# Performance work log

Measured on AMD Instinct MI355X. Metric: run time of the kernel, lower is better.

## Reference

```python
import jax, jax.numpy as jnp
import numpy as np

H = 768       # hidden_size
NH = 12       # num_attention_heads
HD = H // NH  # head_size
FF = 3072     # intermediate_size
EPS = 1e-5


def _layernorm(x, g, b):
    m = jnp.mean(x, axis=-1, keepdims=True)
    v = jnp.var(x, axis=-1, keepdims=True)
    return (x - m) * jax.lax.rsqrt(v + EPS) * g + b


def setup_inputs() -> dict:
    key = jax.random.key(0)
    ks = jax.random.split(key, 12)
    B, Sq, Skv = 8, 1024, 1024
    s = 0.02
    return {
        "freq_hidden_states": jax.random.normal(ks[0], (B, Sq, H), jnp.float32),
        "image_hidden_states": jax.random.normal(ks[1], (B, Skv, H), jnp.float32),
        # attention projections (stored [in, out])
        "Wq": jax.random.normal(ks[2], (H, H), jnp.float32) * s,
        "bq": jnp.zeros((H,), jnp.float32),
        "Wk": jax.random.normal(ks[3], (H, H), jnp.float32) * s,
        "bk": jnp.zeros((H,), jnp.float32),
        "Wv": jax.random.normal(ks[4], (H, H), jnp.float32) * s,
        "bv": jnp.zeros((H,), jnp.float32),
        # layernorms
        "ln_att_g": jnp.ones((H,), jnp.float32),
        "ln_att_b": jnp.zeros((H,), jnp.float32),
        "ln_mlp_g": jnp.ones((H,), jnp.float32),
        "ln_mlp_b": jnp.zeros((H,), jnp.float32),
        # MLP
        "W1": jax.random.normal(ks[5], (H, FF), jnp.float32) * s,
        "b1": jnp.zeros((FF,), jnp.float32),
        "W2": jax.random.normal(ks[6], (FF, H), jnp.float32) * s,
        "b2": jnp.zeros((H,), jnp.float32),
    }


def reference(image_hidden_states, freq_hidden_states, Wq, bq, Wk, bk, Wv, bv,
              ln_att_g, ln_att_b, ln_mlp_g, ln_mlp_b, W1, b1, W2, b2):
    B, Sq, _ = freq_hidden_states.shape
    Skv = image_hidden_states.shape[1]
    # cross-attention: query from freq, key/value from image
    q = (freq_hidden_states @ Wq + bq).reshape(B, Sq, NH, HD)
    k = (image_hidden_states @ Wk + bk).reshape(B, Skv, NH, HD)
    v = (image_hidden_states @ Wv + bv).reshape(B, Skv, NH, HD)
    scores = jnp.einsum("bqhd,bkhd->bhqk", q, k) / jnp.sqrt(jnp.float32(HD))
    probs = jax.nn.softmax(scores, axis=-1)
    ctx = jnp.einsum("bhqk,bkhd->bqhd", probs, v).reshape(B, Sq, H)
    # residual with post-LN on the attention output
    h = freq_hidden_states + _layernorm(ctx, ln_att_g, ln_att_b)
    # MLP + residual with post-LN on the MLP output
    mlp = jax.nn.relu(h @ W1 + b1) @ W2 + b2
    return h + _layernorm(mlp, ln_mlp_g, ln_mlp_b)
```

## Files before the change

kernel.cpp:

```cpp
#include <hip/hip_runtime.h>
#include <hip/hip_bf16.h>

#define H 768
#define NH 12
#define HD 64
#define FF 3072
#define SQ 1024
#define SKV 1024

typedef __hip_bfloat16 bf16;
typedef __attribute__((ext_vector_type(8))) short short8;
typedef __attribute__((ext_vector_type(4))) float f32x4;

__device__ inline void gload16(const void* g, void* l) {
  __builtin_amdgcn_global_load_lds((const __attribute__((address_space(1))) void*)g,
                                   (__attribute__((address_space(3))) void*)l, 16, 0, 0);
}

__device__ inline float bf2f(unsigned short u) {
  unsigned int x = ((unsigned int)u) << 16;
  return __builtin_bit_cast(float, x);
}

__device__ inline void cvt_body(const float* __restrict__ src, bf16* __restrict__ dst, int blk) {
  int i = blk * 256 + threadIdx.x;
  float4 v = ((const float4*)src)[i];
  union { unsigned short u[4]; uint2 q; } o;
  bf16 t0 = __float2bfloat16(v.x); o.u[0] = *(unsigned short*)&t0;
  bf16 t1 = __float2bfloat16(v.y); o.u[1] = *(unsigned short*)&t1;
  bf16 t2 = __float2bfloat16(v.z); o.u[2] = *(unsigned short*)&t2;
  bf16 t3 = __float2bfloat16(v.w); o.u[3] = *(unsigned short*)&t3;
  ((uint2*)dst)[i] = o.q;
}

__device__ inline void trans_body(const float* __restrict__ src, bf16* __restrict__ dst,
                                  int Kd, int Nd, int blk, float* tile ) {
  int ntx = Nd >> 5;
  int n0 = (blk % ntx) << 5, k0 = (blk / ntx) << 5;
  int tx = threadIdx.x & 31, ty = threadIdx.x >> 5;
#pragma unroll
  for (int i = 0; i < 4; ++i)
    tile[(ty + i * 8) * 33 + tx] = src[(size_t)(k0 + ty + i * 8) * Nd + n0 + tx];
  __syncthreads();
#pragma unroll
  for (int i = 0; i < 4; ++i)
    dst[(size_t)(n0 + ty + i * 8) * Kd + k0 + tx] = __float2bfloat16(tile[tx * 33 + ty + i * 8]);
}

__global__ __launch_bounds__(256) void prep(
    const float* freq, const float* image, bf16* freqb, bf16* imageb,
    const float* Wq, const float* Wk, const float* Wv, const float* W1, const float* W2,
    bf16* WTq, bf16* WTk, bf16* WTv, bf16* W1T, bf16* W2T, int c1) {
  __shared__ float tile[32 * 33];
  int b = blockIdx.x;
  if (b < c1) { cvt_body(freq, freqb, b); return; }
  b -= c1;
  if (b < c1) { cvt_body(image, imageb, b); return; }
  b -= c1;
  const int TQ = (H / 32) * (H / 32);
  const int T1 = (FF / 32) * (H / 32);
  if (b < TQ)            { trans_body(Wq, WTq, H, H, b, tile); return; }
  b -= TQ;
  if (b < TQ)            { trans_body(Wk, WTk, H, H, b, tile); return; }
  b -= TQ;
  if (b < TQ)            { trans_body(Wv, WTv, H, H, b, tile); return; }
  b -= TQ;
  if (b < T1)            { trans_body(W1, W1T, H, FF, b, tile); return; }
  b -= T1;
  trans_body(W2, W2T, FF, H, b, tile);
}

template <int EPI, int BN>
__global__ __launch_bounds__(256) void gemm_bt(
    const bf16* __restrict__ A, const bf16* __restrict__ BT,
    const float* __restrict__ bias0, const float* __restrict__ bias1,
    void* __restrict__ out0, void* __restrict__ out1, int M, int N, int K) {
  constexpr int SI = BN / 32;
  constexpr int JF = BN / 32;
  __shared__ __align__(16) bf16 lA[128 * 64];
  __shared__ __align__(16) bf16 lB[BN * 64];
  const int t = threadIdx.x;
  const int lane = t & 63, w = t >> 6;
  const int wr = w >> 1, wc = w & 1;
  const int nt = N / BN;
  const int nwg = gridDim.x;
  int bid = blockIdx.x;
  int logical = ((nwg & 7) == 0) ? ((bid & 7) * (nwg >> 3) + (bid >> 3)) : bid;
  const int m0 = (logical / nt) << 7;
  const int n0 = (logical % nt) * BN;

  const f32x4 fz = {0.f, 0.f, 0.f, 0.f};
  f32x4 acc[4][JF];
#pragma unroll
  for (int i = 0; i < 4; ++i)
#pragma unroll
    for (int j = 0; j < JF; ++j) acc[i][j] = fz;

  for (int kt = 0; kt < K; kt += 64) {
#pragma unroll
    for (int i = 0; i < 4; ++i) {
      int idx = i * 256 + t;
      int row = idx >> 3;
      int chunk = (idx & 7) ^ (row & 7);
      gload16(A + (size_t)(m0 + row) * K + kt + chunk * 8, lA + (size_t)(i * 256 + w * 64) * 8);
    }
#pragma unroll
    for (int i = 0; i < SI; ++i) {
      int idx = i * 256 + t;
      int row = idx >> 3;
      int chunk = (idx & 7) ^ (row & 7);
      gload16(BT + (size_t)(n0 + row) * K + kt + chunk * 8, lB + (size_t)(i * 256 + w * 64) * 8);
    }
    __syncthreads();

    short8 af[2][4], bfv[2][JF];
#pragma unroll
    for (int s = 0; s < 2; ++s) {
#pragma unroll
      for (int i = 0; i < 4; ++i) {
        int ra = wr * 64 + i * 16 + (lane & 15);
        int ca = (s * 4 + (lane >> 4)) ^ (ra & 7);
        af[s][i] = *(const short8*)&lA[ra * 64 + ca * 8];
      }
#pragma unroll
      for (int j = 0; j < JF; ++j) {
        int rb = wc * (BN / 2) + j * 16 + (lane & 15);
        int cb = (s * 4 + (lane >> 4)) ^ (rb & 7);
        bfv[s][j] = *(const short8*)&lB[rb * 64 + cb * 8];
      }
    }
#pragma unroll
    for (int s = 0; s < 2; ++s)
#pragma unroll
      for (int i = 0; i < 4; ++i)
#pragma unroll
        for (int j = 0; j < JF; ++j)
          acc[i][j] = __builtin_amdgcn_mfma_f32_16x16x32_bf16(af[s][i], bfv[s][j], acc[i][j], 0, 0, 0);
    __syncthreads();
  }

#pragma unroll
  for (int i = 0; i < 4; ++i) {
    int mbase = m0 + wr * 64 + i * 16 + ((lane >> 4) << 2);
#pragma unroll
    for (int j = 0; j < JF; ++j) {
      int n = n0 + wc * (BN / 2) + j * 16 + (lane & 15);
#pragma unroll
      for (int r = 0; r < 4; ++r) {
        int m = mbase + r;
        float v = acc[i][j][r];
        if (EPI == 0) {
          v = (v + bias0[n]) * 0.180336880f;
          int hlin = (m >> 10) * NH + (n >> 6);
          ((bf16*)out0)[((size_t)hlin * SQ + (m & 1023)) * HD + (n & 63)] = __float2bfloat16(v);
        } else if (EPI == 1) {
          int sel = (n >= H);
          int nn = n - (sel ? H : 0);
          v += (sel ? bias1 : bias0)[nn];
          int hlin = (m >> 10) * NH + (nn >> 6);
          if (!sel)
            ((bf16*)out0)[((size_t)hlin * SKV + (m & 1023)) * HD + (nn & 63)] = __float2bfloat16(v);
          else
            ((bf16*)out1)[((size_t)hlin * HD + (nn & 63)) * SKV + (m & 1023)] = __float2bfloat16(v);
        } else if (EPI == 2) {
          v += bias0[n];
          v = fmaxf(v, 0.f);
          ((bf16*)out0)[(size_t)m * N + n] = __float2bfloat16(v);
        } else {
          v += bias0[n];
          ((bf16*)out0)[(size_t)m * N + n] = __float2bfloat16(v);
        }
      }
    }
  }
}

__global__ __launch_bounds__(512, 4) void attn_fwd(
    const bf16* __restrict__ Q,
    const bf16* __restrict__ Kg_,
    const bf16* __restrict__ VT,
    bf16* __restrict__ ctx, int nblk) {
  __shared__ __align__(16) bf16 Ks[2][64 * 64];
  __shared__ __align__(16) bf16 Vs[2][64 * 64];
  __shared__ __align__(16) bf16 PQ[8 * 16 * 72];

  const int t = threadIdx.x, lane = t & 63, w = t >> 6;
  int bid = blockIdx.x;
  int logical = ((nblk & 7) == 0) ? (bid & 7) * (nblk >> 3) + (bid >> 3) : bid;
  const int hl = logical >> 3;
  const int q0 = (logical & 7) << 7;
  const bf16* Qg = Q + ((size_t)hl * SQ + q0) * HD;
  const bf16* Kg = Kg_ + (size_t)hl * SKV * HD;
  const bf16* Vg = VT + (size_t)hl * HD * SKV;

#pragma unroll
  for (int rep = 0; rep < 2; ++rep) {
    int idx = rep * 512 + t;
    int row = idx >> 3;
    int chunk = (idx & 7) ^ (row & 7);
    gload16(Qg + (size_t)row * HD + chunk * 8, PQ + (size_t)(rep * 512 + w * 64) * 8);
  }
  {
    int row = t >> 3, chunk = (t & 7) ^ (row & 7);
    gload16(Kg + (size_t)row * HD + chunk * 8, &Ks[0][(size_t)w * 64 * 8]);
    gload16(Vg + (size_t)row * SKV + chunk * 8, &Vs[0][(size_t)w * 64 * 8]);
  }
  __syncthreads();

  short8 aq[2];
#pragma unroll
  for (int s = 0; s < 2; ++s) {
    int row = w * 16 + (lane & 15);
    int chunk = (s * 4 + (lane >> 4)) ^ (row & 7);
    aq[s] = *(const short8*)&PQ[row * 64 + chunk * 8];
  }
  __syncthreads();

  float l_r[4];
#pragma unroll
  for (int r = 0; r < 4; ++r) l_r[r] = 0.f;
  const f32x4 fz = {0.f, 0.f, 0.f, 0.f};
  f32x4 oacc[4];
#pragma unroll
  for (int j = 0; j < 4; ++j) oacc[j] = fz;

  bf16* Pw = PQ + w * (16 * 72);
  const short s1 = (short)0x3F80;
  const short8 ones = {s1, s1, s1, s1, s1, s1, s1, s1};

#pragma unroll 2
  for (int i = 0; i < 16; ++i) {
    const int buf = i & 1;
    if (i < 15) {
      int kvn = (i + 1) << 6;
      int row = t >> 3, chunk = (t & 7) ^ (row & 7);
      gload16(Kg + (size_t)(kvn + row) * HD + chunk * 8, &Ks[buf ^ 1][(size_t)w * 64 * 8]);
      gload16(Vg + (size_t)row * SKV + kvn + chunk * 8, &Vs[buf ^ 1][(size_t)w * 64 * 8]);
    }

    f32x4 sa[4];
#pragma unroll
    for (int n = 0; n < 4; ++n) sa[n] = fz;
    __builtin_amdgcn_s_setprio(1);
#pragma unroll
    for (int s = 0; s < 2; ++s)
#pragma unroll
      for (int n = 0; n < 4; ++n) {
        int rb = n * 16 + (lane & 15);
        int cb = (s * 4 + (lane >> 4)) ^ (rb & 7);
        short8 bk = *(const short8*)&Ks[buf][rb * 64 + cb * 8];
        sa[n] = __builtin_amdgcn_mfma_f32_16x16x32_bf16(aq[s], bk, sa[n], 0, 0, 0);
      }
    __builtin_amdgcn_s_setprio(0);

#pragma unroll
    for (int n = 0; n < 4; ++n)
#pragma unroll
      for (int r = 0; r < 4; ++r)
        Pw[(((lane >> 4) << 2) + r) * 72 + n * 16 + (lane & 15)] =
            __float2bfloat16(exp2f(sa[n][r]));

    f32x4 ld = fz;
    __builtin_amdgcn_s_setprio(1);
#pragma unroll
    for (int kk = 0; kk < 2; ++kk) {
      short8 pa = *(const short8*)&Pw[(lane & 15) * 72 + kk * 32 + ((lane >> 4) << 3)];
      ld = __builtin_amdgcn_mfma_f32_16x16x32_bf16(pa, ones, ld, 0, 0, 0);
#pragma unroll
      for (int j = 0; j < 4; ++j) {
        int rb = j * 16 + (lane & 15);
        int cb = (kk * 4 + (lane >> 4)) ^ (rb & 7);
        short8 bv = *(const short8*)&Vs[buf][rb * 64 + cb * 8];
        oacc[j] = __builtin_amdgcn_mfma_f32_16x16x32_bf16(pa, bv, oacc[j], 0, 0, 0);
      }
    }
    __builtin_amdgcn_s_setprio(0);
#pragma unroll
    for (int r = 0; r < 4; ++r) l_r[r] += ld[r];

    __syncthreads();
  }

  const int b = hl / NH, hh = hl % NH;
  float rl[4];
#pragma unroll
  for (int r = 0; r < 4; ++r) rl[r] = 1.0f / l_r[r];
#pragma unroll
  for (int j = 0; j < 4; ++j)
#pragma unroll
    for (int r = 0; r < 4; ++r) {
      int q = q0 + w * 16 + ((lane >> 4) << 2) + r;
      int d = j * 16 + (lane & 15);
      ctx[((size_t)b * SQ + q) * H + hh * HD + d] = __float2bfloat16(oacc[j][r] * rl[r]);
    }
}

__global__ __launch_bounds__(256) void ln_res(
    const bf16* __restrict__ x, const float* __restrict__ res,
    const float* __restrict__ g, const float* __restrict__ beta,
    float* __restrict__ o32, bf16* __restrict__ ob, int write_b) {
  const int row = blockIdx.x;
  const int t = threadIdx.x;
  float v[4];
  float s = 0.f, s2 = 0.f;
  if (t < 192) {
    ushort4 xv = ((const ushort4*)(x + (size_t)row * H))[t];
    v[0] = bf2f(xv.x); v[1] = bf2f(xv.y); v[2] = bf2f(xv.z); v[3] = bf2f(xv.w);
#pragma unroll
    for (int k = 0; k < 4; ++k) { s += v[k]; s2 += v[k] * v[k]; }
  } else {
#pragma unroll
    for (int k = 0; k < 4; ++k) v[k] = 0.f;
  }
#pragma unroll
  for (int off = 32; off > 0; off >>= 1) {
    s += __shfl_down(s, off);
    s2 += __shfl_down(s2, off);
  }
  __shared__ float red[8];
  if ((t & 63) == 0) { red[t >> 6] = s; red[4 + (t >> 6)] = s2; }
  __syncthreads();
  float st = red[0] + red[1] + red[2] + red[3];
  float s2t = red[4] + red[5] + red[6] + red[7];
  float mean = st * (1.f / 768.f);
  float var = s2t * (1.f / 768.f) - mean * mean;
  float rs = rsqrtf(var + 1e-5f);
  if (t < 192) {
    float4 rv = ((const float4*)(res + (size_t)row * H))[t];
    float4 gv = ((const float4*)g)[t];
    float4 bv = ((const float4*)beta)[t];
    float4 o;
    o.x = rv.x + (v[0] - mean) * rs * gv.x + bv.x;
    o.y = rv.y + (v[1] - mean) * rs * gv.y + bv.y;
    o.z = rv.z + (v[2] - mean) * rs * gv.z + bv.z;
    o.w = rv.w + (v[3] - mean) * rs * gv.w + bv.w;
    ((float4*)(o32 + (size_t)row * H))[t] = o;
    if (write_b) {
      union { unsigned short u[4]; uint2 q; } ob4;
      bf16 b0 = __float2bfloat16(o.x); ob4.u[0] = *(unsigned short*)&b0;
      bf16 b1 = __float2bfloat16(o.y); ob4.u[1] = *(unsigned short*)&b1;
      bf16 b2 = __float2bfloat16(o.z); ob4.u[2] = *(unsigned short*)&b2;
      bf16 b3 = __float2bfloat16(o.w); ob4.u[3] = *(unsigned short*)&b3;
      ((uint2*)(ob + (size_t)row * H))[t] = ob4.q;
    }
  }
}

extern "C" void kernel_launch(void* const* d_in, const int* in_sizes, int n_in,
                              void* d_out, int out_size, void* d_ws, size_t ws_size,
                              hipStream_t stream) {
  const float* freq  = (const float*)d_in[0];
  const float* image = (const float*)d_in[1];
  const float* Wq = (const float*)d_in[2];
  const float* bq = (const float*)d_in[3];
  const float* Wk = (const float*)d_in[4];
  const float* bk = (const float*)d_in[5];
  const float* Wv = (const float*)d_in[6];
  const float* bv = (const float*)d_in[7];
  const float* g1 = (const float*)d_in[8];
  const float* be1 = (const float*)d_in[9];
  const float* g2 = (const float*)d_in[10];
  const float* be2 = (const float*)d_in[11];
  const float* W1 = (const float*)d_in[12];
  const float* b1 = (const float*)d_in[13];
  const float* W2 = (const float*)d_in[14];
  const float* b2 = (const float*)d_in[15];

  const int Bc = in_sizes[0] / (SQ * H);
  const int M = Bc * SQ;

  char* p = (char*)d_ws;
  bf16* W1T = (bf16*)p;  p += (size_t)FF * H * 2;
  bf16* W2T = (bf16*)p;  p += (size_t)H * FF * 2;
  bf16* ctxb = (bf16*)p; p += (size_t)M * H * 2;
  float* h32 = (float*)p; p += (size_t)M * H * 4;
  bf16* hb = (bf16*)p;   p += (size_t)M * H * 2;
  char* U = p;
  bf16* freqb = (bf16*)U;
  bf16* imageb = (bf16*)(U + (size_t)M * H * 2);
  bf16* WTq   = (bf16*)(U + (size_t)2 * M * H * 2);
  bf16* WTkv  = (bf16*)(U + (size_t)2 * M * H * 2 + (size_t)H * H * 2);
  bf16* Qb    = (bf16*)(U + (size_t)2 * M * H * 2 + (size_t)3 * H * H * 2);
  bf16* Kbuf  = (bf16*)((char*)Qb + (size_t)M * H * 2);
  bf16* VTb   = (bf16*)((char*)Kbuf + (size_t)M * H * 2);
  bf16* mlp1  = (bf16*)U;
  bf16* mlp2b = ctxb;

  int c1 = M * H / 1024;
  int nprep = 2 * c1 + 3 * ((H / 32) * (H / 32)) + (FF / 32) * (H / 32) + (H / 32) * (FF / 32);
  prep<<<nprep, 256, 0, stream>>>(freq, image, freqb, imageb,
                                  Wq, Wk, Wv, W1, W2,
                                  WTq, WTkv, WTkv + (size_t)H * H, W1T, W2T, c1);

  gemm_bt<0, 64><<<(M / 128) * (H / 64), 256, 0, stream>>>(freqb, WTq, bq, nullptr, Qb, nullptr, M, H, H);
  gemm_bt<1, 128><<<(M / 128) * (2 * H / 128), 256, 0, stream>>>(imageb, WTkv, bk, bv, Kbuf, VTb, M, 2 * H, H);
  int nblk = Bc * NH * (SQ / 128);
  attn_fwd<<<nblk, 512, 0, stream>>>(Qb, Kbuf, VTb, ctxb, nblk);
  ln_res<<<M, 256, 0, stream>>>(ctxb, freq, g1, be1, h32, hb, 1);
  gemm_bt<2, 128><<<(M / 128) * (FF / 128), 256, 0, stream>>>(hb, W1T, b1, nullptr, mlp1, nullptr, M, FF, H);
  gemm_bt<3, 64><<<(M / 128) * (H / 64), 256, 0, stream>>>(mlp1, W2T, b2, nullptr, mlp2b, nullptr, M, H, FF);
  ln_res<<<M, 256, 0, stream>>>(mlp2b, h32, g2, be2, (float*)d_out, nullptr, 0);
}
```

Before: 246.8 us.

## Rewrite attention with 32x32 MFMA, register-resident P via permlane swap

The attention kernel moves from 8 waves of 16x16x32 MFMA to 4 waves of 32x32x16 MFMA, each wave owning 32 query rows. It computes S^T so the exp'd probabilities can be packed to bf16 with v_cvt_pk and rearranged with v_permlane32_swap into PV operands, removing the LDS round-trip for P. Row sums are accumulated with scalar adds instead of an extra MFMA against ones. This cuts LDS traffic and MFMA instruction count but halves threads per block and raises register pressure per wave.

```diff
diff --git a/kernel.cpp b/kernel.cpp
--- a/kernel.cpp
+++ b/kernel.cpp
@@ -11,6 +11,7 @@
 typedef __hip_bfloat16 bf16;
 typedef __attribute__((ext_vector_type(8))) short short8;
 typedef __attribute__((ext_vector_type(4))) float f32x4;
+typedef __attribute__((ext_vector_type(16))) float f32x16;
 
 __device__ inline void gload16(const void* g, void* l) {
   __builtin_amdgcn_global_load_lds((const __attribute__((address_space(1))) void*)g,
@@ -20,6 +21,12 @@
 __device__ inline float bf2f(unsigned short u) {
   unsigned int x = ((unsigned int)u) << 16;
   return __builtin_bit_cast(float, x);
+}
+
+__device__ inline unsigned int cvtpk(float lo, float hi) {
+  unsigned int r;
+  asm("v_cvt_pk_bf16_f32 %0, %1, %2" : "=v"(r) : "v"(lo), "v"(hi));
+  return r;
 }
 
 __device__ inline void cvt_body(const float* __restrict__ src, bf16* __restrict__ dst, int blk) {
@@ -175,16 +182,17 @@
   }
 }
 
-__global__ __launch_bounds__(512, 4) void attn_fwd(
+__global__ __launch_bounds__(256) void attn_fwd(
     const bf16* __restrict__ Q,
     const bf16* __restrict__ Kg_,
     const bf16* __restrict__ VT,
     bf16* __restrict__ ctx, int nblk) {
+  __shared__ __align__(16) bf16 Qs[128 * 64];
   __shared__ __align__(16) bf16 Ks[2][64 * 64];
   __shared__ __align__(16) bf16 Vs[2][64 * 64];
-  __shared__ __align__(16) bf16 PQ[8 * 16 * 72];
 
   const int t = threadIdx.x, lane = t & 63, w = t >> 6;
+  const int hi = lane >> 5, l31 = lane & 31;
   int bid = blockIdx.x;
   int logical = ((nblk & 7) == 0) ? (bid & 7) * (nblk >> 3) + (bid >> 3) : bid;
   const int hl = logical >> 3;
@@ -194,105 +202,119 @@
   const bf16* Vg = VT + (size_t)hl * HD * SKV;
 
 #pragma unroll
+  for (int rep = 0; rep < 4; ++rep) {
+    int slot = rep * 256 + t;
+    int row = slot >> 3, chunk = (slot & 7) ^ (row & 7);
+    gload16(Qg + (size_t)row * HD + chunk * 8, (char*)Qs + (size_t)slot * 16);
+  }
+#pragma unroll
   for (int rep = 0; rep < 2; ++rep) {
-    int idx = rep * 512 + t;
-    int row = idx >> 3;
-    int chunk = (idx & 7) ^ (row & 7);
-    gload16(Qg + (size_t)row * HD + chunk * 8, PQ + (size_t)(rep * 512 + w * 64) * 8);
-  }
-  {
-    int row = t >> 3, chunk = (t & 7) ^ (row & 7);
-    gload16(Kg + (size_t)row * HD + chunk * 8, &Ks[0][(size_t)w * 64 * 8]);
-    gload16(Vg + (size_t)row * SKV + chunk * 8, &Vs[0][(size_t)w * 64 * 8]);
+    int slot = rep * 256 + t;
+    int row = slot >> 3, chunk = (slot & 7) ^ (row & 7);
+    gload16(Kg + (size_t)row * HD + chunk * 8, (char*)&Ks[0][0] + (size_t)slot * 16);
+    gload16(Vg + (size_t)row * SKV + chunk * 8, (char*)&Vs[0][0] + (size_t)slot * 16);
   }
   __syncthreads();
 
-  short8 aq[2];
-#pragma unroll
-  for (int s = 0; s < 2; ++s) {
-    int row = w * 16 + (lane & 15);
-    int chunk = (s * 4 + (lane >> 4)) ^ (row & 7);
-    aq[s] = *(const short8*)&PQ[row * 64 + chunk * 8];
-  }
-  __syncthreads();
-
-  float l_r[4];
-#pragma unroll
-  for (int r = 0; r < 4; ++r) l_r[r] = 0.f;
-  const f32x4 fz = {0.f, 0.f, 0.f, 0.f};
-  f32x4 oacc[4];
-#pragma unroll
-  for (int j = 0; j < 4; ++j) oacc[j] = fz;
-
-  bf16* Pw = PQ + w * (16 * 72);
-  const short s1 = (short)0x3F80;
-  const short8 ones = {s1, s1, s1, s1, s1, s1, s1, s1};
+  short8 aq[4];
+#pragma unroll
+  for (int ks = 0; ks < 4; ++ks) {
+    int row = w * 32 + l31;
+    int chunk = (ks * 2 + hi) ^ (row & 7);
+    aq[ks] = *(const short8*)&Qs[row * 64 + chunk * 8];
+  }
+
+  f32x16 oa0, oa1;
+#pragma unroll
+  for (int r = 0; r < 16; ++r) { oa0[r] = 0.f; oa1[r] = 0.f; }
+  float ls0 = 0.f, ls1 = 0.f;
 
 #pragma unroll 2
   for (int i = 0; i < 16; ++i) {
     const int buf = i & 1;
     if (i < 15) {
       int kvn = (i + 1) << 6;
-      int row = t >> 3, chunk = (t & 7) ^ (row & 7);
-      gload16(Kg + (size_t)(kvn + row) * HD + chunk * 8, &Ks[buf ^ 1][(size_t)w * 64 * 8]);
-      gload16(Vg + (size_t)row * SKV + kvn + chunk * 8, &Vs[buf ^ 1][(size_t)w * 64 * 8]);
-    }
-
-    f32x4 sa[4];
-#pragma unroll
-    for (int n = 0; n < 4; ++n) sa[n] = fz;
+#pragma unroll
+      for (int rep = 0; rep < 2; ++rep) {
+        int slot = rep * 256 + t;
+        int row = slot >> 3, chunk = (slot & 7) ^ (row & 7);
+        gload16(Kg + (size_t)(kvn + row) * HD + chunk * 8, (char*)&Ks[buf ^ 1][0] + (size_t)slot * 16);
+        gload16(Vg + (size_t)row * SKV + kvn + chunk * 8, (char*)&Vs[buf ^ 1][0] + (size_t)slot * 16);
+      }
+    }
+
+    f32x16 sc0, sc1;
+#pragma unroll
+    for (int r = 0; r < 16; ++r) { sc0[r] = 0.f; sc1[r] = 0.f; }
     __builtin_amdgcn_s_setprio(1);
 #pragma unroll
-    for (int s = 0; s < 2; ++s)
-#pragma unroll
-      for (int n = 0; n < 4; ++n) {
-        int rb = n * 16 + (lane & 15);
-        int cb = (s * 4 + (lane >> 4)) ^ (rb & 7);
-        short8 bk = *(const short8*)&Ks[buf][rb * 64 + cb * 8];
-        sa[n] = __builtin_amdgcn_mfma_f32_16x16x32_bf16(aq[s], bk, sa[n], 0, 0, 0);
+    for (int ks = 0; ks < 4; ++ks) {
+      int c0 = ks * 2 + hi;
+      int r0 = l31;
+      short8 kf0 = *(const short8*)&Ks[buf][r0 * 64 + (c0 ^ (r0 & 7)) * 8];
+      sc0 = __builtin_amdgcn_mfma_f32_32x32x16_bf16(kf0, aq[ks], sc0, 0, 0, 0);
+      int r1 = 32 + l31;
+      short8 kf1 = *(const short8*)&Ks[buf][r1 * 64 + (c0 ^ (r1 & 7)) * 8];
+      sc1 = __builtin_amdgcn_mfma_f32_32x32x16_bf16(kf1, aq[ks], sc1, 0, 0, 0);
+    }
+    __builtin_amdgcn_s_setprio(0);
+
+#pragma unroll
+    for (int r = 0; r < 16; ++r) { sc0[r] = exp2f(sc0[r]); ls0 += sc0[r]; }
+#pragma unroll
+    for (int r = 0; r < 16; ++r) { sc1[r] = exp2f(sc1[r]); ls1 += sc1[r]; }
+
+    short8 pa[4];
+#pragma unroll
+    for (int k4 = 0; k4 < 4; ++k4) {
+      const int base = (k4 & 1) * 8;
+      unsigned int p0, p1, qq0, qq1;
+      if (k4 & 2) {
+        p0 = cvtpk(sc1[base + 0], sc1[base + 1]);
+        p1 = cvtpk(sc1[base + 2], sc1[base + 3]);
+        qq0 = cvtpk(sc1[base + 4], sc1[base + 5]);
+        qq1 = cvtpk(sc1[base + 6], sc1[base + 7]);
+      } else {
+        p0 = cvtpk(sc0[base + 0], sc0[base + 1]);
+        p1 = cvtpk(sc0[base + 2], sc0[base + 3]);
+        qq0 = cvtpk(sc0[base + 4], sc0[base + 5]);
+        qq1 = cvtpk(sc0[base + 6], sc0[base + 7]);
       }
+      asm volatile("v_permlane32_swap_b32 %0, %1" : "+v"(p0), "+v"(qq0));
+      asm volatile("v_permlane32_swap_b32 %0, %1" : "+v"(p1), "+v"(qq1));
+      union { unsigned int u[4]; short8 s8; } pu;
+      pu.u[0] = p0; pu.u[1] = p1; pu.u[2] = qq0; pu.u[3] = qq1;
+      pa[k4] = pu.s8;
+    }
+
+    __builtin_amdgcn_s_setprio(1);
+#pragma unroll
+    for (int k4 = 0; k4 < 4; ++k4) {
+      int cc = k4 * 2 + hi;
+      int r0 = l31;
+      short8 vf0 = *(const short8*)&Vs[buf][r0 * 64 + (cc ^ (r0 & 7)) * 8];
+      oa0 = __builtin_amdgcn_mfma_f32_32x32x16_bf16(pa[k4], vf0, oa0, 0, 0, 0);
+      int r1 = 32 + l31;
+      short8 vf1 = *(const short8*)&Vs[buf][r1 * 64 + (cc ^ (r1 & 7)) * 8];
+      oa1 = __builtin_amdgcn_mfma_f32_32x32x16_bf16(pa[k4], vf1, oa1, 0, 0, 0);
+    }
     __builtin_amdgcn_s_setprio(0);
 
-#pragma unroll
-    for (int n = 0; n < 4; ++n)
-#pragma unroll
-      for (int r = 0; r < 4; ++r)
-        Pw[(((lane >> 4) << 2) + r) * 72 + n * 16 + (lane & 15)] =
-            __float2bfloat16(exp2f(sa[n][r]));
-
-    f32x4 ld = fz;
-    __builtin_amdgcn_s_setprio(1);
-#pragma unroll
-    for (int kk = 0; kk < 2; ++kk) {
-      short8 pa = *(const short8*)&Pw[(lane & 15) * 72 + kk * 32 + ((lane >> 4) << 3)];
-      ld = __builtin_amdgcn_mfma_f32_16x16x32_bf16(pa, ones, ld, 0, 0, 0);
-#pragma unroll
-      for (int j = 0; j < 4; ++j) {
-        int rb = j * 16 + (lane & 15);
-        int cb = (kk * 4 + (lane >> 4)) ^ (rb & 7);
-        short8 bv = *(const short8*)&Vs[buf][rb * 64 + cb * 8];
-        oacc[j] = __builtin_amdgcn_mfma_f32_16x16x32_bf16(pa, bv, oacc[j], 0, 0, 0);
-      }
-    }
-    __builtin_amdgcn_s_setprio(0);
-#pragma unroll
-    for (int r = 0; r < 4; ++r) l_r[r] += ld[r];
-
     __syncthreads();
   }
 
+  float lt = (ls0 + ls1) + __shfl_xor(ls0 + ls1, 32);
+  float rlq = 1.0f / lt;
   const int b = hl / NH, hh = hl % NH;
-  float rl[4];
-#pragma unroll
-  for (int r = 0; r < 4; ++r) rl[r] = 1.0f / l_r[r];
-#pragma unroll
-  for (int j = 0; j < 4; ++j)
-#pragma unroll
-    for (int r = 0; r < 4; ++r) {
-      int q = q0 + w * 16 + ((lane >> 4) << 2) + r;
-      int d = j * 16 + (lane & 15);
-      ctx[((size_t)b * SQ + q) * H + hh * HD + d] = __float2bfloat16(oacc[j][r] * rl[r]);
-    }
+  bf16* outp = ctx + ((size_t)b * SQ + q0 + w * 32) * H + hh * HD;
+#pragma unroll
+  for (int r = 0; r < 16; ++r) {
+    int qo = (r & 3) + 8 * (r >> 2) + 4 * hi;
+    float rv = __shfl(rlq, qo);
+    bf16* rowp = outp + (size_t)qo * H;
+    rowp[l31]      = __float2bfloat16(oa0[r] * rv);
+    rowp[32 + l31] = __float2bfloat16(oa1[r] * rv);
+  }
 }
 
 __global__ __launch_bounds__(256) void ln_res(
@@ -395,7 +417,7 @@
   gemm_bt<0, 64><<<(M / 128) * (H / 64), 256, 0, stream>>>(freqb, WTq, bq, nullptr, Qb, nullptr, M, H, H);
   gemm_bt<1, 128><<<(M / 128) * (2 * H / 128), 256, 0, stream>>>(imageb, WTkv, bk, bv, Kbuf, VTb, M, 2 * H, H);
   int nblk = Bc * NH * (SQ / 128);
-  attn_fwd<<<nblk, 512, 0, stream>>>(Qb, Kbuf, VTb, ctxb, nblk);
+  attn_fwd<<<nblk, 256, 0, stream>>>(Qb, Kbuf, VTb, ctxb, nblk);
   ln_res<<<M, 256, 0, stream>>>(ctxb, freq, g1, be1, h32, hb, 1);
   gemm_bt<2, 128><<<(M / 128) * (FF / 128), 256, 0, stream>>>(hb, W1T, b1, nullptr, mlp1, nullptr, M, FF, H);
   gemm_bt<3, 64><<<(M / 128) * (H / 64), 256, 0, stream>>>(mlp1, W2T, b2, nullptr, mlp2b, nullptr, M, H, FF);
```

Measured after the change: 249.6 us. About the same (+1.1%).
